# Optimization experiments

Measured on AMD Instinct MI355X. Metric: run time of the kernel, lower is better.

The kernel has to match this reference:

```python
import jax, jax.numpy as jnp
import numpy as np

B, S, E = 4, 1024, 1280
H = 16
D = E // H  # 80


def rotate_half(x):
    x1, x2 = jnp.split(x, 2, axis=-1)
    return jnp.concatenate([-x2, x1], axis=-1)


def setup_inputs() -> dict:
    key = jax.random.key(0)
    ks = jax.random.split(key, 12)
    sc = 0.02
    x = jax.random.normal(ks[0], (B, S, E), dtype=jnp.float32)
    # variable per-item sequence lengths (each <= S), cumulative
    lens = np.array([1024, 896, 768, 640], dtype=np.int32)
    cu_seqlens = jnp.asarray(np.concatenate([[0], np.cumsum(lens)]), dtype=jnp.int32)
    # rotary cos/sin for positions 0..S-1, head_dim D
    inv_freq = 1.0 / (10000.0 ** (np.arange(0, D, 2, dtype=np.float32) / D))
    t = np.arange(S, dtype=np.float32)
    freqs = np.outer(t, inv_freq)               # [S, D/2]
    emb = np.concatenate([freqs, freqs], axis=-1)  # [S, D]
    cos = jnp.asarray(np.cos(emb), dtype=jnp.float32)
    sin = jnp.asarray(np.sin(emb), dtype=jnp.float32)
    wq = jax.random.normal(ks[1], (E, E), dtype=jnp.float32) * sc
    bq = jax.random.normal(ks[2], (E,), dtype=jnp.float32) * sc
    wk = jax.random.normal(ks[3], (E, E), dtype=jnp.float32) * sc
    bk = jax.random.normal(ks[4], (E,), dtype=jnp.float32) * sc
    wv = jax.random.normal(ks[5], (E, E), dtype=jnp.float32) * sc
    bv = jax.random.normal(ks[6], (E,), dtype=jnp.float32) * sc
    wo = jax.random.normal(ks[7], (E, E), dtype=jnp.float32) * sc
    bo = jax.random.normal(ks[8], (E,), dtype=jnp.float32) * sc
    return {"x": x, "cu_seqlens": cu_seqlens, "cos": cos, "sin": sin,
            "wq": wq, "bq": bq, "wk": wk, "bk": bk, "wv": wv, "bv": bv,
            "wo": wo, "bo": bo}


def reference(x, cu_seqlens, cos, sin, wq, bq, wk, bk, wv, bv, wo, bo):
    b, s, e = x.shape
    h, d = H, D
    # QKV projections (nn.Linear: x @ W^T + b)
    q = (x @ wq.T + bq).reshape(b, s, h, d)
    k = (x @ wk.T + bk).reshape(b, s, h, d)
    v = (x @ wv.T + bv).reshape(b, s, h, d)
    # rotary embedding (apply_rotary_pos_emb, 'normal')
    c = cos[None, :, None, :]  # [1, s, 1, d]
    sn = sin[None, :, None, :]
    q = q * c + rotate_half(q) * sn
    k = k * c + rotate_half(k) * sn
    # patch attention mask from cu_seqlens (flatten_batch=False):
    # token i attends to token j iff i < len_b and j < len_b
    seq_lens = cu_seqlens[1:] - cu_seqlens[:-1]          # [b]
    idx = jnp.arange(s)
    valid = idx[None, :] < seq_lens[:, None]             # [b, s]
    mask = valid[:, None, :, None] & valid[:, None, None, :]  # [b, 1, s, s]
    # SDPA, non-causal
    scale = 1.0 / jnp.sqrt(jnp.asarray(d, dtype=q.dtype))
    scores = jnp.einsum("bqhd,bkhd->bhqk", q, k) * scale
    scores = jnp.where(mask, scores, jnp.asarray(-1e9, dtype=scores.dtype))
    attn = jax.nn.softmax(scores, axis=-1)
    out = jnp.einsum("bhqk,bkhd->bqhd", attn, v)         # [b, s, h, d]
    out = out.reshape(b, s, e)
    # output projection
    return out @ wo.T + bo
```

## Files before the change

### kernel.cpp

```cpp
#include <hip/hip_runtime.h>
#include <hip/hip_bf16.h>

#define B_ 4
#define S_ 1024
#define E_ 1280
#define H_ 16
#define D_ 80
#define M_ (B_*S_)

typedef __hip_bfloat16 bf16;
using bf16x8 = __attribute__((ext_vector_type(8))) short;
using f32x4  = __attribute__((ext_vector_type(4))) float;

__device__ __forceinline__ float b2f(bf16 x){ return __bfloat162float(x); }
__device__ __forceinline__ bf16  f2b(float x){ return __float2bfloat16(x); }
__device__ __forceinline__ void  stf(float* p, float v){ *p = v; }
__device__ __forceinline__ void  stf(bf16*  p, float v){ *p = f2b(v); }

__device__ __forceinline__ void gload_lds16(const void* g, void* l) {
    __builtin_amdgcn_global_load_lds(
        (const __attribute__((address_space(1))) unsigned int*)g,
        (__attribute__((address_space(3))) unsigned int*)l, 16, 0, 0);
}

__global__ __launch_bounds__(256) void cvt_kernel(
    const float* __restrict__ s0, const float* __restrict__ s1,
    const float* __restrict__ s2, const float* __restrict__ s3,
    const float* __restrict__ s4,
    bf16* __restrict__ d0, bf16* __restrict__ d1, bf16* __restrict__ d2,
    bf16* __restrict__ d3, bf16* __restrict__ d4,
    int n0, int n1)
{
    const float* s; bf16* d; int n;
    switch (blockIdx.y) {
        case 0: s = s0; d = d0; n = n0; break;
        case 1: s = s1; d = d1; n = n1; break;
        case 2: s = s2; d = d2; n = n1; break;
        case 3: s = s3; d = d3; n = n1; break;
        default: s = s4; d = d4; n = n1; break;
    }
    int i = (blockIdx.x * 256 + threadIdx.x) * 8;
    if (i >= n) return;
    float4 a = *(const float4*)(s + i);
    float4 b = *(const float4*)(s + i + 4);
    bf16 t[8];
    t[0]=f2b(a.x); t[1]=f2b(a.y); t[2]=f2b(a.z); t[3]=f2b(a.w);
    t[4]=f2b(b.x); t[5]=f2b(b.y); t[6]=f2b(b.z); t[7]=f2b(b.w);
    *(uint4*)(d + i) = *(const uint4*)t;
}

template<typename TC, bool VT_OUT>
__global__ __launch_bounds__(256) void mfma_gemm_bt(
    const bf16* __restrict__ A,
    const bf16* __restrict__ W0, const bf16* __restrict__ W1, const bf16* __restrict__ W2,
    const float* __restrict__ b0, const float* __restrict__ b1, const float* __restrict__ b2,
    TC* __restrict__ C0, TC* __restrict__ C1, TC* __restrict__ C2,
    int K, int N, int ntiles)
{
    const int mat = blockIdx.y / ntiles;
    const int bn  = (blockIdx.y % ntiles) * 128;
    const int bm  = blockIdx.x * 128;
    const bf16* W; const float* bias; TC* C;
    if (mat == 0)      { W = W0; bias = b0; C = C0; }
    else if (mat == 1) { W = W1; bias = b1; C = C1; }
    else               { W = W2; bias = b2; C = C2; }

    __shared__ bf16 As[2][128][32];
    __shared__ bf16 Ws[2][128][32];

    const int tid  = threadIdx.x;
    const int lane = tid & 63;
    const int wv   = tid >> 6;
    const int wm   = (wv & 1) * 64;
    const int wn   = (wv >> 1) * 64;
    const int srow = wv * 16 + (lane >> 2);
    const int scol = (lane & 3) * 8;

    f32x4 acc[4][4] = {};

    for (int k0 = 0; k0 < K; k0 += 64) {
        __syncthreads();
        #pragma unroll
        for (int p = 0; p < 2; p++) {
            const int kc = k0 + p*32 + scol;
            gload_lds16(A + (size_t)(bm + srow)      * K + kc, &As[p][wv*16][0]);
            gload_lds16(A + (size_t)(bm + 64 + srow) * K + kc, &As[p][64 + wv*16][0]);
            gload_lds16(W + (size_t)(bn + srow)      * K + kc, &Ws[p][wv*16][0]);
            gload_lds16(W + (size_t)(bn + 64 + srow) * K + kc, &Ws[p][64 + wv*16][0]);
        }
        __syncthreads();

        const int fr = lane & 15;
        const int kq = (lane >> 4) * 8;
        #pragma unroll
        for (int p = 0; p < 2; p++) {
            bf16x8 af[4], wf[4];
            #pragma unroll
            for (int t = 0; t < 4; t++) {
                af[t] = *(const bf16x8*)&As[p][wm + t*16 + fr][kq];
                wf[t] = *(const bf16x8*)&Ws[p][wn + t*16 + fr][kq];
            }
            #pragma unroll
            for (int mt = 0; mt < 4; mt++)
                #pragma unroll
                for (int nt = 0; nt < 4; nt++)
                    acc[mt][nt] = __builtin_amdgcn_mfma_f32_16x16x32_bf16(
                        af[mt], wf[nt], acc[mt][nt], 0, 0, 0);
        }
    }

    const int col_l = lane & 15;
    const int row_l = (lane >> 4) * 4;

    if (VT_OUT && mat == 2) {
        const int btok = bm >> 10;
        const int keyb = (bm & 1023) + wm + row_l;
        #pragma unroll
        for (int nt = 0; nt < 4; nt++) {
            const int n = bn + wn + nt*16 + col_l;
            const float bv = bias[n];
            const int hh = n / 80, dd = n % 80;
            bf16* vbase = (bf16*)C + ((size_t)(btok*H_ + hh)*D_ + dd)*S_ + keyb;
            #pragma unroll
            for (int mt = 0; mt < 4; mt++) {
                union { bf16 h[4]; uint2 u; } t4;
                #pragma unroll
                for (int r = 0; r < 4; r++) t4.h[r] = f2b(acc[mt][nt][r] + bv);
                *(uint2*)&vbase[mt*16] = t4.u;
            }
        }
    } else {
        #pragma unroll
        for (int nt = 0; nt < 4; nt++) {
            const int n = bn + wn + nt*16 + col_l;
            const float bv = bias[n];
            #pragma unroll
            for (int mt = 0; mt < 4; mt++) {
                #pragma unroll
                for (int r = 0; r < 4; r++) {
                    const int m = bm + wm + mt*16 + row_l + r;
                    stf(&C[(size_t)m * N + n], acc[mt][nt][r] + bv);
                }
            }
        }
    }
}

__device__ __forceinline__ void rope8(const bf16* lo, const bf16* hi,
                                      const float* cp, const float* sp,
                                      float mul, uint4* out_lo, uint4* out_hi)
{
    union { uint4 u; bf16 h[8]; } li, hi_, lo_o, hi_o;
    li.u  = *(const uint4*)lo;
    hi_.u = *(const uint4*)hi;
    #pragma unroll
    for (int u = 0; u < 8; u++) {
        float x1 = b2f(li.h[u]), x2 = b2f(hi_.h[u]);
        float c = cp[u], s = sp[u];
        lo_o.h[u] = f2b((x1*c - x2*s) * mul);
        hi_o.h[u] = f2b((x2*c + x1*s) * mul);
    }
    *out_lo = lo_o.u;
    *out_hi = hi_o.u;
}

__global__ __launch_bounds__(256, 4) void attn_mfma(
    const bf16* __restrict__ q, const bf16* __restrict__ k, const bf16* __restrict__ vt,
    const int* __restrict__ cu, const float* __restrict__ cosp, const float* __restrict__ sinp,
    bf16* __restrict__ o)
{
    __shared__ __align__(16) char smem[38144];
    bf16* Qs  = (bf16*)smem;
    bf16* Ks  = (bf16*)(smem + 13312);
    bf16* VTs = (bf16*)(smem + 26624);

    const int L  = blockIdx.x;
    const int qt = L >> 6;
    const int g  = L & 63;
    const int b  = g >> 4;
    const int h  = g & 15;

    const int tid = threadIdx.x;
    const int lane = tid & 63, wv = tid >> 6;
    const int quad = lane >> 4, l15 = lane & 15;
    const int q0 = qt * 64;
    const int len = cu[b + 1] - cu[b];
    const float scale = 0.11180339887498949f;

    const bool uniformq = (q0 >= len);
    const bool cleanlen = ((len & 63) == 0);
    const int  ktiles   = uniformq ? 16 : (cleanlen ? (len >> 6) : 16);
    const bool domask   = !uniformq && !cleanlen;

    bf16* PT = (bf16*)(smem + wv * 2304);

    bf16x8 qf[3];
    if (!uniformq) {
        #pragma unroll
        for (int i = 0; i < 2; i++) {
            int c = tid + i * 256;
            if (c < 320) {
                int row = c / 5, pc = c % 5;
                int s = q0 + row;
                const bf16* src = q + (size_t)(b*S_ + s)*E_ + h*D_ + pc*8;
                uint4 olo, ohi;
                rope8(src, src + 40, cosp + s*D_ + pc*8, sinp + s*D_ + pc*8, scale, &olo, &ohi);
                *(uint4*)&Qs[row*104 + pc*8]      = olo;
                *(uint4*)&Qs[row*104 + (pc+5)*8]  = ohi;
            }
        }
        if (tid < 128) {
            uint4 z = make_uint4(0,0,0,0);
            int row = tid >> 1, c8 = 10 + (tid & 1);
            *(uint4*)&Qs[row*104 + c8*8] = z;
            *(uint4*)&Ks[row*104 + c8*8] = z;
        }
        __syncthreads();
        #pragma unroll
        for (int ks = 0; ks < 3; ks++)
            qf[ks] = *(const bf16x8*)&Qs[(wv*16 + l15)*104 + ks*32 + quad*8];
    } else {
        const bf16 one = f2b(1.0f);
        #pragma unroll
        for (int nt = 0; nt < 4; nt++)
            #pragma unroll
            for (int r = 0; r < 4; r++)
                PT[(quad*4 + r)*72 + nt*16 + l15] = one;
    }

    float m_r[4], l_r[4];
    #pragma unroll
    for (int r = 0; r < 4; r++) { m_r[r] = -1e30f; l_r[r] = 0.f; }
    f32x4 o_acc[5] = {};

    const bool q_full = (q0 + 64) <= len;

    for (int kt = 0; kt < ktiles; kt++) {
        __syncthreads();
        if (!uniformq) {
            #pragma unroll
            for (int i = 0; i < 2; i++) {
                int c = tid + i * 256;
                if (c < 320) {
                    int row = c / 5, pc = c % 5;
                    int s = kt*64 + row;
                    const bf16* src = k + (size_t)(b*S_ + s)*E_ + h*D_ + pc*8;
                    uint4 olo, ohi;
                    rope8(src, src + 40, cosp + s*D_ + pc*8, sinp + s*D_ + pc*8, 1.0f, &olo, &ohi);
                    *(uint4*)&Ks[row*104 + pc*8]      = olo;
                    *(uint4*)&Ks[row*104 + (pc+5)*8]  = ohi;
                }
            }
        }
        #pragma unroll
        for (int i = 0; i < 3; i++) {
            int c = tid + i * 256;
            if (c < 640) {
                int d = c >> 3, kc = c & 7;
                *(uint4*)&VTs[d*72 + kc*8] =
                    *(const uint4*)(vt + ((size_t)(b*H_ + h)*D_ + d)*S_ + kt*64 + kc*8);
            }
        }
        __syncthreads();

        if (!uniformq) {
            f32x4 s4[4];
            #pragma unroll
            for (int nt = 0; nt < 4; nt++) {
                f32x4 a0 = {};
                #pragma unroll
                for (int ks = 0; ks < 3; ks++) {
                    bf16x8 kf = *(const bf16x8*)&Ks[(nt*16 + l15)*104 + ks*32 + quad*8];
                    a0 = __builtin_amdgcn_mfma_f32_16x16x32_bf16(qf[ks], kf, a0, 0, 0, 0);
                }
                s4[nt] = a0;
            }

            float sv[4][4];
            if (!domask || (q_full && (kt*64 + 64) <= len)) {
                #pragma unroll
                for (int r = 0; r < 4; r++)
                    #pragma unroll
                    for (int nt = 0; nt < 4; nt++)
                        sv[nt][r] = s4[nt][r];
            } else {
                bool vk[4];
                #pragma unroll
                for (int nt = 0; nt < 4; nt++) vk[nt] = (kt*64 + nt*16 + l15) < len;
                #pragma unroll
                for (int r = 0; r < 4; r++) {
                    const bool vq = (q0 + wv*16 + quad*4 + r) < len;
                    #pragma unroll
                    for (int nt = 0; nt < 4; nt++)
                        sv[nt][r] = (vq && vk[nt]) ? s4[nt][r] : -1e9f;
                }
            }
            float rmax[4];
            #pragma unroll
            for (int r = 0; r < 4; r++)
                rmax[r] = fmaxf(fmaxf(sv[0][r], sv[1][r]), fmaxf(sv[2][r], sv[3][r]));
            #pragma unroll
            for (int st = 1; st < 16; st <<= 1)
                #pragma unroll
                for (int r = 0; r < 4; r++)
                    rmax[r] = fmaxf(rmax[r], __shfl_xor(rmax[r], st, 64));
            float mnew[4], alpha[4], rsum[4], p[4][4];
            #pragma unroll
            for (int r = 0; r < 4; r++) {
                mnew[r]  = fmaxf(m_r[r], rmax[r]);
                alpha[r] = __expf(m_r[r] - mnew[r]);
                float a = 0.f;
                #pragma unroll
                for (int nt = 0; nt < 4; nt++) { p[nt][r] = __expf(sv[nt][r] - mnew[r]); a += p[nt][r]; }
                rsum[r] = a;
            }
            #pragma unroll
            for (int st = 1; st < 16; st <<= 1)
                #pragma unroll
                for (int r = 0; r < 4; r++)
                    rsum[r] += __shfl_xor(rsum[r], st, 64);
            #pragma unroll
            for (int r = 0; r < 4; r++) {
                l_r[r] = l_r[r] * alpha[r] + rsum[r];
                m_r[r] = mnew[r];
            }
            #pragma unroll
            for (int dt = 0; dt < 5; dt++)
                #pragma unroll
                for (int r = 0; r < 4; r++)
                    o_acc[dt][r] *= alpha[r];
            #pragma unroll
            for (int nt = 0; nt < 4; nt++)
                #pragma unroll
                for (int r = 0; r < 4; r++)
                    PT[(quad*4 + r)*72 + nt*16 + l15] = f2b(p[nt][r]);
        }

        bf16x8 pa[2];
        #pragma unroll
        for (int ks = 0; ks < 2; ks++)
            pa[ks] = *(const bf16x8*)&PT[l15*72 + ks*32 + quad*8];
        #pragma unroll
        for (int dt = 0; dt < 5; dt++) {
            #pragma unroll
            for (int ks = 0; ks < 2; ks++) {
                bf16x8 vf = *(const bf16x8*)&VTs[(dt*16 + l15)*72 + ks*32 + quad*8];
                o_acc[dt] = __builtin_amdgcn_mfma_f32_16x16x32_bf16(pa[ks], vf, o_acc[dt], 0, 0, 0);
            }
        }
    }

    #pragma unroll
    for (int r = 0; r < 4; r++) {
        const float inv = uniformq ? (1.0f / 1024.0f) : (1.0f / l_r[r]);
        size_t row_g = (size_t)(b*S_ + q0 + wv*16 + quad*4 + r);
        #pragma unroll
        for (int dt = 0; dt < 5; dt++)
            o[row_g*E_ + h*D_ + dt*16 + l15] = f2b(o_acc[dt][r] * inv);
    }
}

extern "C" void kernel_launch(void* const* d_in, const int* in_sizes, int n_in,
                              void* d_out, int out_size, void* d_ws, size_t ws_size,
                              hipStream_t stream)
{
    const float* x    = (const float*)d_in[0];
    const int*   cu   = (const int*)  d_in[1];
    const float* cosp = (const float*)d_in[2];
    const float* sinp = (const float*)d_in[3];
    const float* wq   = (const float*)d_in[4];
    const float* bq   = (const float*)d_in[5];
    const float* wk   = (const float*)d_in[6];
    const float* bk   = (const float*)d_in[7];
    const float* wv   = (const float*)d_in[8];
    const float* bv   = (const float*)d_in[9];
    const float* wo   = (const float*)d_in[10];
    const float* bo   = (const float*)d_in[11];
    float* out = (float*)d_out;

    bf16* q   = (bf16*)d_ws;
    bf16* kk  = q   + (size_t)M_ * E_;
    bf16* vt  = kk  + (size_t)M_ * E_;
    bf16* ao  = vt  + (size_t)M_ * E_;
    bf16* xb  = ao  + (size_t)M_ * E_;
    bf16* wqb = xb  + (size_t)M_ * E_;
    bf16* wkb = wqb + (size_t)E_ * E_;
    bf16* wvb = wkb + (size_t)E_ * E_;
    bf16* wob = wvb + (size_t)E_ * E_;

    cvt_kernel<<<dim3(2560, 5), 256, 0, stream>>>(
        x, wq, wk, wv, wo, xb, wqb, wkb, wvb, wob, M_*E_, E_*E_);

    mfma_gemm_bt<bf16, true><<<dim3(M_/128, 30), 256, 0, stream>>>(
        xb, wqb, wkb, wvb, bq, bk, bv, q, kk, vt, E_, E_, 10);

    attn_mfma<<<1024, 256, 0, stream>>>(q, kk, vt, cu, cosp, sinp, ao);

    mfma_gemm_bt<float, false><<<dim3(M_/128, 10), 256, 0, stream>>>(
        ao, wob, wob, wob, bo, bo, bo, out, out, out, E_, E_, 10);
}
```

Measured before the change: 272.0 us.

## Hoist RoPE into separate kernel and read K/V fragments directly from global

RoPE is moved out of the attention kernel into a standalone in-place pass over Q and K, so each K tile is no longer re-rotated by all 16 query-tile blocks. The attention kernel then drops its shared-memory staging of Q, K and V and the block-wide barriers, loading MFMA fragments straight from global (relying on L2/L1 reuse). The smaller LDS footprint allows higher occupancy (launch bounds raised to 8), and block indices are remapped so blocks sharing a head are scheduled near each other. In exchange it adds a kernel launch and an extra read/write pass over Q/K, and it issues uncoalesced, strided global loads per lane.

New measurement: 461.4 us. 69.6% more time.

```diff
diff --git a/kernel.cpp b/kernel.cpp
--- a/kernel.cpp
+++ b/kernel.cpp
@@ -164,61 +164,60 @@
     *out_hi = hi_o.u;
 }
 
-__global__ __launch_bounds__(256, 4) void attn_mfma(
+__global__ __launch_bounds__(256) void rope_kernel(
+    bf16* __restrict__ qp, bf16* __restrict__ kp,
+    const float* __restrict__ cosp, const float* __restrict__ sinp)
+{
+    int idx = blockIdx.x * 256 + threadIdx.x;
+    const int NT = M_ * H_ * 5;
+    bf16* base; float mul;
+    if (idx < NT) { base = qp; mul = 0.11180339887498949f; }
+    else         { base = kp; mul = 1.0f; idx -= NT; }
+    const int row = idx / 80;
+    const int rem = idx - row * 80;
+    const int h   = rem / 5;
+    const int pc  = rem - h * 5;
+    const int s   = row & (S_ - 1);
+    bf16* p = base + (size_t)row * E_ + h * D_ + pc * 8;
+    const float* cp = cosp + s * D_ + pc * 8;
+    const float* sp = sinp + s * D_ + pc * 8;
+    uint4 olo, ohi;
+    rope8(p, p + 40, cp, sp, mul, &olo, &ohi);
+    *(uint4*)p        = olo;
+    *(uint4*)(p + 40) = ohi;
+}
+
+__global__ __launch_bounds__(256, 8) void attn_mfma(
     const bf16* __restrict__ q, const bf16* __restrict__ k, const bf16* __restrict__ vt,
-    const int* __restrict__ cu, const float* __restrict__ cosp, const float* __restrict__ sinp,
-    bf16* __restrict__ o)
-{
-    __shared__ __align__(16) char smem[38144];
-    bf16* Qs  = (bf16*)smem;
-    bf16* Ks  = (bf16*)(smem + 13312);
-    bf16* VTs = (bf16*)(smem + 26624);
-
-    const int L  = blockIdx.x;
-    const int qt = L >> 6;
-    const int g  = L & 63;
+    const int* __restrict__ cu, bf16* __restrict__ o)
+{
+    __shared__ __align__(16) bf16 PTs[4][16 * 72];
+
+    const int n  = blockIdx.x;
+    const int g  = (n & 7) * 8 + (n >> 7);
+    const int qt = (n >> 3) & 15;
     const int b  = g >> 4;
     const int h  = g & 15;
 
-    const int tid = threadIdx.x;
+    const int tid  = threadIdx.x;
     const int lane = tid & 63, wv = tid >> 6;
     const int quad = lane >> 4, l15 = lane & 15;
-    const int q0 = qt * 64;
-    const int len = cu[b + 1] - cu[b];
-    const float scale = 0.11180339887498949f;
+    const int q0   = qt * 64;
+    const int len  = cu[b + 1] - cu[b];
 
     const bool uniformq = (q0 >= len);
     const bool cleanlen = ((len & 63) == 0);
     const int  ktiles   = uniformq ? 16 : (cleanlen ? (len >> 6) : 16);
     const bool domask   = !uniformq && !cleanlen;
 
-    bf16* PT = (bf16*)(smem + wv * 2304);
-
-    bf16x8 qf[3];
+    bf16* PT = &PTs[wv][0];
+
+    bf16x8 qf[3] = {};
     if (!uniformq) {
-        #pragma unroll
-        for (int i = 0; i < 2; i++) {
-            int c = tid + i * 256;
-            if (c < 320) {
-                int row = c / 5, pc = c % 5;
-                int s = q0 + row;
-                const bf16* src = q + (size_t)(b*S_ + s)*E_ + h*D_ + pc*8;
-                uint4 olo, ohi;
-                rope8(src, src + 40, cosp + s*D_ + pc*8, sinp + s*D_ + pc*8, scale, &olo, &ohi);
-                *(uint4*)&Qs[row*104 + pc*8]      = olo;
-                *(uint4*)&Qs[row*104 + (pc+5)*8]  = ohi;
-            }
-        }
-        if (tid < 128) {
-            uint4 z = make_uint4(0,0,0,0);
-            int row = tid >> 1, c8 = 10 + (tid & 1);
-            *(uint4*)&Qs[row*104 + c8*8] = z;
-            *(uint4*)&Ks[row*104 + c8*8] = z;
-        }
-        __syncthreads();
-        #pragma unroll
-        for (int ks = 0; ks < 3; ks++)
-            qf[ks] = *(const bf16x8*)&Qs[(wv*16 + l15)*104 + ks*32 + quad*8];
+        const bf16* qrow = q + (size_t)(b*S_ + q0 + wv*16 + l15)*E_ + h*D_ + quad*8;
+        qf[0] = *(const bf16x8*)(qrow);
+        qf[1] = *(const bf16x8*)(qrow + 32);
+        if (quad < 2) qf[2] = *(const bf16x8*)(qrow + 64);
     } else {
         const bf16 one = f2b(1.0f);
         #pragma unroll
@@ -235,44 +234,24 @@
 
     const bool q_full = (q0 + 64) <= len;
 
+    const bf16* kbase0 = k  + (size_t)(b*S_ + l15)*E_ + h*D_ + quad*8;
+    const bf16* vbase0 = vt + ((size_t)(b*H_ + h)*D_ + l15)*S_ + quad*8;
+
     for (int kt = 0; kt < ktiles; kt++) {
-        __syncthreads();
-        if (!uniformq) {
-            #pragma unroll
-            for (int i = 0; i < 2; i++) {
-                int c = tid + i * 256;
-                if (c < 320) {
-                    int row = c / 5, pc = c % 5;
-                    int s = kt*64 + row;
-                    const bf16* src = k + (size_t)(b*S_ + s)*E_ + h*D_ + pc*8;
-                    uint4 olo, ohi;
-                    rope8(src, src + 40, cosp + s*D_ + pc*8, sinp + s*D_ + pc*8, 1.0f, &olo, &ohi);
-                    *(uint4*)&Ks[row*104 + pc*8]      = olo;
-                    *(uint4*)&Ks[row*104 + (pc+5)*8]  = ohi;
-                }
-            }
-        }
-        #pragma unroll
-        for (int i = 0; i < 3; i++) {
-            int c = tid + i * 256;
-            if (c < 640) {
-                int d = c >> 3, kc = c & 7;
-                *(uint4*)&VTs[d*72 + kc*8] =
-                    *(const uint4*)(vt + ((size_t)(b*H_ + h)*D_ + d)*S_ + kt*64 + kc*8);
-            }
-        }
-        __syncthreads();
-
         if (!uniformq) {
             f32x4 s4[4];
+            const bf16* kb = kbase0 + (size_t)kt * 64 * E_;
             #pragma unroll
             for (int nt = 0; nt < 4; nt++) {
+                const bf16* krow = kb + (size_t)nt * 16 * E_;
+                bf16x8 kf0 = *(const bf16x8*)(krow);
+                bf16x8 kf1 = *(const bf16x8*)(krow + 32);
+                bf16x8 kf2 = {};
+                if (quad < 2) kf2 = *(const bf16x8*)(krow + 64);
                 f32x4 a0 = {};
-                #pragma unroll
-                for (int ks = 0; ks < 3; ks++) {
-                    bf16x8 kf = *(const bf16x8*)&Ks[(nt*16 + l15)*104 + ks*32 + quad*8];
-                    a0 = __builtin_amdgcn_mfma_f32_16x16x32_bf16(qf[ks], kf, a0, 0, 0, 0);
-                }
+                a0 = __builtin_amdgcn_mfma_f32_16x16x32_bf16(qf[0], kf0, a0, 0, 0, 0);
+                a0 = __builtin_amdgcn_mfma_f32_16x16x32_bf16(qf[1], kf1, a0, 0, 0, 0);
+                a0 = __builtin_amdgcn_mfma_f32_16x16x32_bf16(qf[2], kf2, a0, 0, 0, 0);
                 s4[nt] = a0;
             }
 
@@ -337,14 +316,14 @@
         }
 
         bf16x8 pa[2];
-        #pragma unroll
-        for (int ks = 0; ks < 2; ks++)
-            pa[ks] = *(const bf16x8*)&PT[l15*72 + ks*32 + quad*8];
+        pa[0] = *(const bf16x8*)&PT[l15*72 + quad*8];
+        pa[1] = *(const bf16x8*)&PT[l15*72 + 32 + quad*8];
+        const bf16* vb = vbase0 + kt * 64;
         #pragma unroll
         for (int dt = 0; dt < 5; dt++) {
             #pragma unroll
             for (int ks = 0; ks < 2; ks++) {
-                bf16x8 vf = *(const bf16x8*)&VTs[(dt*16 + l15)*72 + ks*32 + quad*8];
+                bf16x8 vf = *(const bf16x8*)(vb + (size_t)dt*16*S_ + ks*32);
                 o_acc[dt] = __builtin_amdgcn_mfma_f32_16x16x32_bf16(pa[ks], vf, o_acc[dt], 0, 0, 0);
             }
         }
@@ -394,7 +373,9 @@
     mfma_gemm_bt<bf16, true><<<dim3(M_/128, 30), 256, 0, stream>>>(
         xb, wqb, wkb, wvb, bq, bk, bv, q, kk, vt, E_, E_, 10);
 
-    attn_mfma<<<1024, 256, 0, stream>>>(q, kk, vt, cu, cosp, sinp, ao);
+    rope_kernel<<<2560, 256, 0, stream>>>(q, kk, cosp, sinp);
+
+    attn_mfma<<<1024, 256, 0, stream>>>(q, kk, vt, cu, ao);
 
     mfma_gemm_bt<float, false><<<dim3(M_/128, 10), 256, 0, stream>>>(
         ao, wob, wob, wob, bo, bo, bo, out, out, out, E_, E_, 10);
```
